# Kernel tuning notes

Hardware: AMD Instinct MI355X
Metric: run time of the kernel (lower is better)

## Reference

```python
import jax, jax.numpy as jnp
import numpy as np

TOP_K = 2


def setup_inputs() -> dict:
    key = jax.random.key(0)
    ks = jax.random.split(key, 5)
    B, S, D, F, E = 4, 2048, 1024, 2048, 8
    sd = 1.0 / np.sqrt(D)
    sf = 1.0 / np.sqrt(F)
    return {
        "hidden_states": jax.random.normal(ks[0], (B, S, D), jnp.float32),
        "router_w1": jax.random.normal(ks[1], (D, 128), jnp.float32) * sd,
        "router_w2": jax.random.normal(ks[2], (128, E), jnp.float32) * (1.0 / np.sqrt(128)),
        "W1": jax.random.normal(ks[3], (E, D, F), jnp.float32) * sd,
        "W2": jax.random.normal(ks[4], (E, F, D), jnp.float32) * sf,
    }


def reference(hidden_states, router_w1, router_w2, W1, W2):
    B, S, D = hidden_states.shape
    E = W1.shape[0]
    # --- Router: MLP -> softmax -> top-k -> renormalize ---
    router_logits = jax.nn.silu(hidden_states @ router_w1) @ router_w2  # (B,S,E)
    router_probs = jax.nn.softmax(router_logits, axis=-1)
    top_vals, top_idx = jax.lax.top_k(router_probs, TOP_K)  # (B,S,K)
    routing_weights = top_vals / jnp.sum(top_vals, axis=-1, keepdims=True)

    # --- Dispatch/combine as dense combine-weight matrix (faithful to
    # weighted scatter-add combine in _grouped_expert_forward) ---
    T = B * S
    x = hidden_states.reshape(T, D)
    idx = top_idx.reshape(T, TOP_K)
    w = routing_weights.reshape(T, TOP_K).astype(hidden_states.dtype)
    combine = jnp.zeros((T, E), hidden_states.dtype).at[
        jnp.arange(T)[:, None], idx
    ].add(w)  # (T,E)

    # --- Per-expert FFN on all tokens, then weighted combine ---
    h = jax.nn.silu(jnp.einsum("td,edf->tef", x, W1))  # (T,E,F)
    expert_out = jnp.einsum("tef,efd->ted", h, W2)      # (T,E,D)
    out = jnp.einsum("te,ted->td", combine, expert_out)
    return out.reshape(B, S, D)
```

## Files before the change

### kernel.cpp

```cpp
#include <hip/hip_runtime.h>
#include <hip/hip_bf16.h>
#include <math.h>

#define T_TOK 8192
#define E_NUM 8
#define GAP_TAU 2e-3f

typedef __attribute__((ext_vector_type(8))) short short8;
typedef __attribute__((ext_vector_type(4))) float floatx4;

__device__ __forceinline__ unsigned short f2bf(float f) {
  unsigned int u = __builtin_bit_cast(unsigned int, f);
  u += 0x7fffu + ((u >> 16) & 1u);
  return (unsigned short)(u >> 16);
}

__device__ __forceinline__ void async16(const unsigned short* g, unsigned short* l) {
  __builtin_amdgcn_global_load_lds(
      (const __attribute__((address_space(1))) void*)g,
      (__attribute__((address_space(3))) void*)l, 16, 0, 0);
}

__global__ __launch_bounds__(256) void router_fp32_kernel(
    const float* __restrict__ x, const float* __restrict__ rw1,
    const float* __restrict__ rw2,
    int* __restrict__ tok_top, float* __restrict__ tok_w,
    int* __restrict__ fix_list, int* __restrict__ fix_cnt) {
  __shared__ __align__(16) float xs[8][1024];
  __shared__ float ph[128][8];
  __shared__ float hs[8][129];
  __shared__ float ls[8][8];
  const int t = threadIdx.x;
  const int tok0 = blockIdx.x * 8;

  {
    const float4* xsrc = (const float4*)(x + (size_t)tok0 * 1024);
    float4* xd = (float4*)&xs[0][0];
#pragma unroll
    for (int i = 0; i < 8; ++i) xd[t + i * 256] = xsrc[t + i * 256];
  }
  __syncthreads();

  const int j = t & 127, h = t >> 7;
  float acc[8];
#pragma unroll
  for (int tt = 0; tt < 8; ++tt) acc[tt] = 0.f;

  const int dbeg = h * 512, dend = dbeg + 512;
#pragma unroll 2
  for (int d0 = dbeg; d0 < dend; d0 += 4) {
    float w0 = rw1[(d0 + 0) * 128 + j];
    float w1 = rw1[(d0 + 1) * 128 + j];
    float w2 = rw1[(d0 + 2) * 128 + j];
    float w3 = rw1[(d0 + 3) * 128 + j];
    float4 xv[8];
#pragma unroll
    for (int tt = 0; tt < 8; ++tt) xv[tt] = *(const float4*)&xs[tt][d0];
#pragma unroll
    for (int tt = 0; tt < 8; ++tt) {
      acc[tt] = fmaf(xv[tt].x, w0, acc[tt]);
      acc[tt] = fmaf(xv[tt].y, w1, acc[tt]);
      acc[tt] = fmaf(xv[tt].z, w2, acc[tt]);
      acc[tt] = fmaf(xv[tt].w, w3, acc[tt]);
    }
  }
  if (h == 1) {
#pragma unroll
    for (int tt = 0; tt < 8; ++tt) ph[j][tt] = acc[tt];
  }
  __syncthreads();
  if (h == 0) {
#pragma unroll
    for (int tt = 0; tt < 8; ++tt) {
      float a = acc[tt] + ph[j][tt];
      hs[tt][j] = a / (1.f + expf(-a));
    }
  }
  __syncthreads();
  if (t < 64) {
    int tt = t >> 3, e = t & 7;
    float l = 0.f;
#pragma unroll 4
    for (int jj = 0; jj < 128; ++jj) l = fmaf(hs[tt][jj], rw2[jj * 8 + e], l);
    ls[tt][e] = l;
  }
  __syncthreads();
  if (t < 8) {
    int tt = t;
    float l[8];
#pragma unroll
    for (int e = 0; e < 8; ++e) l[e] = ls[tt][e];
    int i0 = 0;
#pragma unroll
    for (int e = 1; e < 8; ++e) if (l[e] > l[i0]) i0 = e;
    int i1 = (i0 == 0) ? 1 : 0;
#pragma unroll
    for (int e = 0; e < 8; ++e) if (e != i0 && l[e] > l[i1]) i1 = e;
    float v2 = -3.4e38f;
#pragma unroll
    for (int e = 0; e < 8; ++e) if (e != i0 && e != i1 && l[e] > v2) v2 = l[e];
    float gap = l[i1] - v2;
    float p = expf(l[i1] - l[i0]);
    float w0 = 1.f / (1.f + p);
    int tok = tok0 + tt;
    tok_top[2 * tok] = i0; tok_top[2 * tok + 1] = i1;
    tok_w[2 * tok] = w0;   tok_w[2 * tok + 1] = 1.f - w0;
    if (gap < GAP_TAU) { int pos = atomicAdd(fix_cnt, 1); fix_list[pos] = tok; }
  }
}

__global__ __launch_bounds__(256) void router_fix_kernel(
    const float* __restrict__ x, const float* __restrict__ rw1,
    const float* __restrict__ rw2, const int* __restrict__ fix_list,
    const int* __restrict__ fix_cnt,
    int* __restrict__ tok_top, float* __restrict__ tok_w) {
  __shared__ __align__(16) float xs[1024];
  __shared__ double red[128];
  __shared__ double hs[128];
  __shared__ double ls[8];
  const int t = threadIdx.x;
  const int nfix = *fix_cnt;
  for (int it = blockIdx.x; it < nfix; it += gridDim.x) {
    int tok = fix_list[it];
    ((float4*)xs)[t] = ((const float4*)(x + (size_t)tok * 1024))[t];
    __syncthreads();
    const int j = t & 127, h = t >> 7;
    double a0 = 0, a1 = 0, a2 = 0, a3 = 0;
    const int dbeg = h * 512;
    for (int d0 = dbeg; d0 < dbeg + 512; d0 += 4) {
      a0 = fma((double)xs[d0 + 0], (double)rw1[(d0 + 0) * 128 + j], a0);
      a1 = fma((double)xs[d0 + 1], (double)rw1[(d0 + 1) * 128 + j], a1);
      a2 = fma((double)xs[d0 + 2], (double)rw1[(d0 + 2) * 128 + j], a2);
      a3 = fma((double)xs[d0 + 3], (double)rw1[(d0 + 3) * 128 + j], a3);
    }
    double a = (a0 + a1) + (a2 + a3);
    if (h == 1) red[j] = a;
    __syncthreads();
    if (h == 0) {
      double s = a + red[j];
      hs[j] = s / (1.0 + exp(-s));
    }
    __syncthreads();
    if (t < 8) {
      int e = t;
      double l = 0;
      for (int jj = 0; jj < 128; ++jj) l = fma(hs[jj], (double)rw2[jj * 8 + e], l);
      ls[e] = l;
    }
    __syncthreads();
    if (t == 0) {
      double l[8];
#pragma unroll
      for (int e = 0; e < 8; ++e) l[e] = ls[e];
      int i0 = 0;
#pragma unroll
      for (int e = 1; e < 8; ++e) if (l[e] > l[i0]) i0 = e;
      int i1 = (i0 == 0) ? 1 : 0;
#pragma unroll
      for (int e = 0; e < 8; ++e) if (e != i0 && l[e] > l[i1]) i1 = e;
      double p = exp(l[i1] - l[i0]);
      double w0 = 1.0 / (1.0 + p);
      tok_top[2 * tok] = i0; tok_top[2 * tok + 1] = i1;
      tok_w[2 * tok] = (float)w0; tok_w[2 * tok + 1] = (float)(1.0 - w0);
    }
    __syncthreads();
  }
}

__global__ __launch_bounds__(256) void scatter_kernel(
    const int* __restrict__ tok_top, const float* __restrict__ tok_w,
    int* __restrict__ cnt, int* __restrict__ tid_list, float* __restrict__ tw_list) {
  __shared__ int hist[8], run[8];
  const int t = threadIdx.x;
  if (t < 8) hist[t] = 0;
  __syncthreads();
  const int tok = blockIdx.x * 256 + t;
  const int e0 = tok_top[2 * tok], e1 = tok_top[2 * tok + 1];
  atomicAdd(&hist[e0], 1);
  atomicAdd(&hist[e1], 1);
  __syncthreads();
  if (t < 8) run[t] = atomicAdd(&cnt[t], hist[t]);
  __syncthreads();
  int p0 = atomicAdd(&run[e0], 1);
  tid_list[e0 * T_TOK + p0] = tok; tw_list[e0 * T_TOK + p0] = tok_w[2 * tok];
  int p1 = atomicAdd(&run[e1], 1);
  tid_list[e1 * T_TOK + p1] = tok; tw_list[e1 * T_TOK + p1] = tok_w[2 * tok + 1];
}

__global__ void prefix_kernel(const int* __restrict__ cnt, int* __restrict__ base) {
  if (threadIdx.x == 0 && blockIdx.x == 0) {
    int s = 0;
    for (int e = 0; e < E_NUM; ++e) { base[e] = s; s += cnt[e]; }
  }
}

__global__ __launch_bounds__(256) void convert_x_kernel(const float* __restrict__ in,
                                                        unsigned short* __restrict__ out) {
  size_t i = ((size_t)blockIdx.x * 256 + threadIdx.x) * 4;
  float4 v = *(const float4*)(in + i);
  ushort4 o;
  o.x = f2bf(v.x); o.y = f2bf(v.y); o.z = f2bf(v.z); o.w = f2bf(v.w);
  *(ushort4*)(out + i) = o;
}

__global__ __launch_bounds__(256) void transpose_bf16_kernel(
    const float* __restrict__ in, unsigned short* __restrict__ out, int R, int C) {
  __shared__ unsigned short tile[64][65];
  const int e = blockIdx.z;
  const int r0 = blockIdx.y * 64, c0 = blockIdx.x * 64;
  const float* src = in + (size_t)e * R * C;
  unsigned short* dst = out + (size_t)e * R * C;
  const int t = threadIdx.x;
  const int cc = (t & 15) * 4;
#pragma unroll
  for (int p = 0; p < 4; ++p) {
    int r = p * 16 + (t >> 4);
    float4 v = *(const float4*)(src + (size_t)(r0 + r) * C + c0 + cc);
    tile[cc + 0][r] = f2bf(v.x);
    tile[cc + 1][r] = f2bf(v.y);
    tile[cc + 2][r] = f2bf(v.z);
    tile[cc + 3][r] = f2bf(v.w);
  }
  __syncthreads();
#pragma unroll
  for (int p = 0; p < 4; ++p) {
    int fr = p * 16 + (t >> 4);
    ushort4 o;
    o.x = tile[fr][cc + 0]; o.y = tile[fr][cc + 1];
    o.z = tile[fr][cc + 2]; o.w = tile[fr][cc + 3];
    *(ushort4*)(dst + (size_t)(c0 + fr) * R + r0 + cc) = o;
  }
}

__global__ __launch_bounds__(256) void gemm1_kernel(
    const unsigned short* __restrict__ xb,
    const unsigned short* __restrict__ w1t,
    const int* __restrict__ cnt, const int* __restrict__ base,
    const int* __restrict__ tid_list,
    unsigned short* __restrict__ h_buf) {
  const int e = blockIdx.z;
  const int m0 = blockIdx.y * 128;
  const int n0 = blockIdx.x * 128;
  const int count = cnt[e];
  if (m0 >= count) return;
  const int bs = base[e];

  __shared__ __align__(16) unsigned short As[128 * 64];
  __shared__ __align__(16) unsigned short Bs[128 * 64];

  const int t = threadIdx.x;
  const int wv = t >> 6, lane = t & 63;
  const int quad = lane >> 4, lr = lane & 15;
  const int wm = (wv & 1) * 64, wn = (wv >> 1) * 64;
  const int lr8 = lane >> 3, lc8 = lane & 7;
  const int chunk = lc8 ^ lr8;

  const unsigned short* aptr[4];
  const unsigned short* bptr[4];
#pragma unroll
  for (int q = 0; q < 4; ++q) {
    int ar = m0 + wv * 32 + q * 8 + lr8;
    int ai = ar < count ? ar : count - 1;
    int tok = tid_list[e * T_TOK + ai];
    aptr[q] = xb + (size_t)tok * 1024 + chunk * 8;
    int br = n0 + wv * 32 + q * 8 + lr8;
    bptr[q] = w1t + ((size_t)e * 2048 + br) * 1024 + chunk * 8;
  }
  unsigned short* aldsb = &As[wv * 2048];
  unsigned short* bldsb = &Bs[wv * 2048];

  floatx4 zero = {0.f, 0.f, 0.f, 0.f};
  floatx4 acc[4][4];
#pragma unroll
  for (int i = 0; i < 4; ++i)
#pragma unroll
    for (int j = 0; j < 4; ++j) acc[i][j] = zero;

  for (int k0 = 0; k0 < 1024; k0 += 64) {
    __syncthreads();
#pragma unroll
    for (int q = 0; q < 4; ++q) {
      async16(aptr[q] + k0, aldsb + q * 512);
      async16(bptr[q] + k0, bldsb + q * 512);
    }
    __syncthreads();
#pragma unroll
    for (int ks = 0; ks < 2; ++ks) {
      short8 af[4], bfv[4];
#pragma unroll
      for (int i = 0; i < 4; ++i) {
        int r = wm + i * 16 + lr;
        int pc = (ks * 4 + quad) ^ (lr & 7);
        af[i] = *(const short8*)&As[r * 64 + pc * 8];
      }
#pragma unroll
      for (int j = 0; j < 4; ++j) {
        int r = wn + j * 16 + lr;
        int pc = (ks * 4 + quad) ^ (lr & 7);
        bfv[j] = *(const short8*)&Bs[r * 64 + pc * 8];
      }
#pragma unroll
      for (int i = 0; i < 4; ++i)
#pragma unroll
        for (int j = 0; j < 4; ++j)
          acc[i][j] = __builtin_amdgcn_mfma_f32_16x16x32_bf16(af[i], bfv[j], acc[i][j], 0, 0, 0);
    }
  }

#pragma unroll
  for (int i = 0; i < 4; ++i) {
#pragma unroll
    for (int r = 0; r < 4; ++r) {
      int grow = m0 + wm + i * 16 + quad * 4 + r;
      if (grow < count) {
        size_t rowoff = (size_t)(bs + grow) * 2048;
#pragma unroll
        for (int j = 0; j < 4; ++j) {
          float v = acc[i][j][r];
          float s = v / (1.0f + __expf(-v));
          h_buf[rowoff + n0 + wn + j * 16 + lr] = f2bf(s);
        }
      }
    }
  }
}

__global__ __launch_bounds__(256) void gemm2_kernel(
    const unsigned short* __restrict__ h_buf,
    const unsigned short* __restrict__ w2t,
    const int* __restrict__ cnt, const int* __restrict__ base,
    const int* __restrict__ tid_list, const float* __restrict__ tw_list,
    float* __restrict__ out) {
  const int e = blockIdx.z;
  const int m0 = blockIdx.y * 128;
  const int n0 = blockIdx.x * 128;
  const int count = cnt[e];
  if (m0 >= count) return;
  const int bs = base[e];

  __shared__ __align__(16) unsigned short As[128 * 64];
  __shared__ __align__(16) unsigned short Bs[128 * 64];

  const int t = threadIdx.x;
  const int wv = t >> 6, lane = t & 63;
  const int quad = lane >> 4, lr = lane & 15;
  const int wm = (wv & 1) * 64, wn = (wv >> 1) * 64;
  const int lr8 = lane >> 3, lc8 = lane & 7;
  const int chunk = lc8 ^ lr8;

  const unsigned short* aptr[4];
  const unsigned short* bptr[4];
#pragma unroll
  for (int q = 0; q < 4; ++q) {
    int ar = m0 + wv * 32 + q * 8 + lr8;
    int ai = ar < count ? ar : count - 1;
    aptr[q] = h_buf + (size_t)(bs + ai) * 2048 + chunk * 8;
    int br = n0 + wv * 32 + q * 8 + lr8;
    bptr[q] = w2t + ((size_t)e * 1024 + br) * 2048 + chunk * 8;
  }
  unsigned short* aldsb = &As[wv * 2048];
  unsigned short* bldsb = &Bs[wv * 2048];

  floatx4 zero = {0.f, 0.f, 0.f, 0.f};
  floatx4 acc[4][4];
#pragma unroll
  for (int i = 0; i < 4; ++i)
#pragma unroll
    for (int j = 0; j < 4; ++j) acc[i][j] = zero;

  for (int k0 = 0; k0 < 2048; k0 += 64) {
    __syncthreads();
#pragma unroll
    for (int q = 0; q < 4; ++q) {
      async16(aptr[q] + k0, aldsb + q * 512);
      async16(bptr[q] + k0, bldsb + q * 512);
    }
    __syncthreads();
#pragma unroll
    for (int ks = 0; ks < 2; ++ks) {
      short8 af[4], bfv[4];
#pragma unroll
      for (int i = 0; i < 4; ++i) {
        int r = wm + i * 16 + lr;
        int pc = (ks * 4 + quad) ^ (lr & 7);
        af[i] = *(const short8*)&As[r * 64 + pc * 8];
      }
#pragma unroll
      for (int j = 0; j < 4; ++j) {
        int r = wn + j * 16 + lr;
        int pc = (ks * 4 + quad) ^ (lr & 7);
        bfv[j] = *(const short8*)&Bs[r * 64 + pc * 8];
      }
#pragma unroll
      for (int i = 0; i < 4; ++i)
#pragma unroll
        for (int j = 0; j < 4; ++j)
          acc[i][j] = __builtin_amdgcn_mfma_f32_16x16x32_bf16(af[i], bfv[j], acc[i][j], 0, 0, 0);
    }
  }

#pragma unroll
  for (int i = 0; i < 4; ++i) {
#pragma unroll
    for (int r = 0; r < 4; ++r) {
      int grow = m0 + wm + i * 16 + quad * 4 + r;
      if (grow < count) {
        int tok = tid_list[e * T_TOK + grow];
        float w = tw_list[e * T_TOK + grow];
        size_t rowoff = (size_t)tok * 1024;
#pragma unroll
        for (int j = 0; j < 4; ++j) {
          unsafeAtomicAdd(&out[rowoff + n0 + wn + j * 16 + lr], acc[i][j][r] * w);
        }
      }
    }
  }
}

extern "C" void kernel_launch(void* const* d_in, const int* in_sizes, int n_in,
                              void* d_out, int out_size, void* d_ws, size_t ws_size,
                              hipStream_t stream) {
  const float* x   = (const float*)d_in[0];
  const float* rw1 = (const float*)d_in[1];
  const float* rw2 = (const float*)d_in[2];
  const float* W1  = (const float*)d_in[3];
  const float* W2  = (const float*)d_in[4];
  float* out = (float*)d_out;

  char* ws = (char*)d_ws;
  int*            cnt      = (int*)(ws + 0);
  int*            base     = (int*)(ws + 64);
  int*            fix_cnt  = (int*)(ws + 128);
  int*            tid_list = (int*)(ws + 512);
  float*          tw_list  = (float*)(ws + 262656);
  unsigned short* xb       = (unsigned short*)(ws + 524800);
  unsigned short* w1t      = (unsigned short*)(ws + 17302016);
  unsigned short* w2t      = (unsigned short*)(ws + 50856448);
  unsigned short* hbuf     = (unsigned short*)(ws + 84410880);
  int*            tok_top  = (int*)(ws + 151519744);
  float*          tok_w    = (float*)(ws + 151585280);
  int*            fix_list = (int*)(ws + 151650816);

  hipMemsetAsync(d_out, 0, (size_t)T_TOK * 1024 * 4, stream);
  hipMemsetAsync(ws, 0, 192, stream);

  hipLaunchKernelGGL(router_fp32_kernel, dim3(1024), dim3(256), 0, stream,
                     x, rw1, rw2, tok_top, tok_w, fix_list, fix_cnt);
  hipLaunchKernelGGL(router_fix_kernel, dim3(128), dim3(256), 0, stream,
                     x, rw1, rw2, fix_list, fix_cnt, tok_top, tok_w);
  hipLaunchKernelGGL(scatter_kernel, dim3(32), dim3(256), 0, stream,
                     tok_top, tok_w, cnt, tid_list, tw_list);
  hipLaunchKernelGGL(prefix_kernel, dim3(1), dim3(1), 0, stream, cnt, base);
  hipLaunchKernelGGL(convert_x_kernel, dim3(8192), dim3(256), 0, stream, x, xb);
  hipLaunchKernelGGL(transpose_bf16_kernel, dim3(32, 16, 8), dim3(256), 0, stream,
                     W1, w1t, 1024, 2048);
  hipLaunchKernelGGL(transpose_bf16_kernel, dim3(16, 32, 8), dim3(256), 0, stream,
                     W2, w2t, 2048, 1024);
  hipLaunchKernelGGL(gemm1_kernel, dim3(16, 64, 8), dim3(256), 0, stream,
                     xb, w1t, cnt, base, tid_list, hbuf);
  hipLaunchKernelGGL(gemm2_kernel, dim3(8, 64, 8), dim3(256), 0, stream,
                     hbuf, w2t, cnt, base, tid_list, tw_list, out);
}
```

Measured before the change: 565.5 us.

## Fuse bf16 conversion into router and compact GEMM grids with XCD-aware tile mapping

The fp32-to-bf16 conversion of the activations moves into the router kernel, which already loads each token row, so the separate conversion kernel and its extra read of x go away. Both grouped GEMMs switch from a 3D grid padded to the worst case per expert to a 1D grid. Each block derives its expert, M tile and N tile from a prefix sum of per-expert tile counts. The low 3 bits of the block index select an XCD band, so blocks that share tiles sit on the same XCD for L2 reuse. This removes many empty blocks that exit at once. The cost is a small per-block prefix computation, and the fixed grid sizes (2176 and 1088) must cover the total number of tiles.

```diff
diff --git a/kernel.cpp b/kernel.cpp
--- a/kernel.cpp
+++ b/kernel.cpp
@@ -21,11 +21,34 @@
       (__attribute__((address_space(3))) void*)l, 16, 0, 0);
 }
 
+__device__ __forceinline__ bool tile_map(int flat, const int* cnt, int nt_log2,
+                                         int& e, int& m0, int& n0) {
+  const int xcd = flat & 7;
+  const int idx = flat >> 3;
+  int mtp[E_NUM + 1];
+  mtp[0] = 0;
+#pragma unroll
+  for (int q = 0; q < E_NUM; ++q) mtp[q + 1] = mtp[q] + ((cnt[q] + 127) >> 7);
+  const int MT = mtp[E_NUM];
+  const int band = (MT + 7) >> 3;
+  const int i = idx >> nt_log2;
+  if (i >= band) return false;
+  const int g = xcd * band + i;
+  if (g >= MT) return false;
+  e = 0;
+#pragma unroll
+  for (int q = 0; q < E_NUM - 1; ++q) if (g >= mtp[q + 1]) e = q + 1;
+  m0 = (g - mtp[e]) << 7;
+  n0 = (idx & ((1 << nt_log2) - 1)) << 7;
+  return true;
+}
+
 __global__ __launch_bounds__(256) void router_fp32_kernel(
     const float* __restrict__ x, const float* __restrict__ rw1,
     const float* __restrict__ rw2,
     int* __restrict__ tok_top, float* __restrict__ tok_w,
-    int* __restrict__ fix_list, int* __restrict__ fix_cnt) {
+    int* __restrict__ fix_list, int* __restrict__ fix_cnt,
+    unsigned short* __restrict__ xb) {
   __shared__ __align__(16) float xs[8][1024];
   __shared__ float ph[128][8];
   __shared__ float hs[8][129];
@@ -36,8 +59,15 @@
   {
     const float4* xsrc = (const float4*)(x + (size_t)tok0 * 1024);
     float4* xd = (float4*)&xs[0][0];
-#pragma unroll
-    for (int i = 0; i < 8; ++i) xd[t + i * 256] = xsrc[t + i * 256];
+    ushort4* xbd = (ushort4*)(xb + (size_t)tok0 * 1024);
+#pragma unroll
+    for (int i = 0; i < 8; ++i) {
+      float4 v = xsrc[t + i * 256];
+      xd[t + i * 256] = v;
+      ushort4 o;
+      o.x = f2bf(v.x); o.y = f2bf(v.y); o.z = f2bf(v.z); o.w = f2bf(v.w);
+      xbd[t + i * 256] = o;
+    }
   }
   __syncthreads();
 
@@ -194,15 +224,6 @@
   }
 }
 
-__global__ __launch_bounds__(256) void convert_x_kernel(const float* __restrict__ in,
-                                                        unsigned short* __restrict__ out) {
-  size_t i = ((size_t)blockIdx.x * 256 + threadIdx.x) * 4;
-  float4 v = *(const float4*)(in + i);
-  ushort4 o;
-  o.x = f2bf(v.x); o.y = f2bf(v.y); o.z = f2bf(v.z); o.w = f2bf(v.w);
-  *(ushort4*)(out + i) = o;
-}
-
 __global__ __launch_bounds__(256) void transpose_bf16_kernel(
     const float* __restrict__ in, unsigned short* __restrict__ out, int R, int C) {
   __shared__ unsigned short tile[64][65];
@@ -238,11 +259,9 @@
     const int* __restrict__ cnt, const int* __restrict__ base,
     const int* __restrict__ tid_list,
     unsigned short* __restrict__ h_buf) {
-  const int e = blockIdx.z;
-  const int m0 = blockIdx.y * 128;
-  const int n0 = blockIdx.x * 128;
+  int e, m0, n0;
+  if (!tile_map(blockIdx.x, cnt, 4, e, m0, n0)) return;
   const int count = cnt[e];
-  if (m0 >= count) return;
   const int bs = base[e];
 
   __shared__ __align__(16) unsigned short As[128 * 64];
@@ -331,11 +350,9 @@
     const int* __restrict__ cnt, const int* __restrict__ base,
     const int* __restrict__ tid_list, const float* __restrict__ tw_list,
     float* __restrict__ out) {
-  const int e = blockIdx.z;
-  const int m0 = blockIdx.y * 128;
-  const int n0 = blockIdx.x * 128;
+  int e, m0, n0;
+  if (!tile_map(blockIdx.x, cnt, 3, e, m0, n0)) return;
   const int count = cnt[e];
-  if (m0 >= count) return;
   const int bs = base[e];
 
   __shared__ __align__(16) unsigned short As[128 * 64];
@@ -445,19 +462,18 @@
   hipMemsetAsync(ws, 0, 192, stream);
 
   hipLaunchKernelGGL(router_fp32_kernel, dim3(1024), dim3(256), 0, stream,
-                     x, rw1, rw2, tok_top, tok_w, fix_list, fix_cnt);
+                     x, rw1, rw2, tok_top, tok_w, fix_list, fix_cnt, xb);
   hipLaunchKernelGGL(router_fix_kernel, dim3(128), dim3(256), 0, stream,
                      x, rw1, rw2, fix_list, fix_cnt, tok_top, tok_w);
   hipLaunchKernelGGL(scatter_kernel, dim3(32), dim3(256), 0, stream,
                      tok_top, tok_w, cnt, tid_list, tw_list);
   hipLaunchKernelGGL(prefix_kernel, dim3(1), dim3(1), 0, stream, cnt, base);
-  hipLaunchKernelGGL(convert_x_kernel, dim3(8192), dim3(256), 0, stream, x, xb);
   hipLaunchKernelGGL(transpose_bf16_kernel, dim3(32, 16, 8), dim3(256), 0, stream,
                      W1, w1t, 1024, 2048);
   hipLaunchKernelGGL(transpose_bf16_kernel, dim3(16, 32, 8), dim3(256), 0, stream,
                      W2, w2t, 2048, 1024);
-  hipLaunchKernelGGL(gemm1_kernel, dim3(16, 64, 8), dim3(256), 0, stream,
+  hipLaunchKernelGGL(gemm1_kernel, dim3(2176), dim3(256), 0, stream,
                      xb, w1t, cnt, base, tid_list, hbuf);
-  hipLaunchKernelGGL(gemm2_kernel, dim3(8, 64, 8), dim3(256), 0, stream,
+  hipLaunchKernelGGL(gemm2_kernel, dim3(1088), dim3(256), 0, stream,
                      hbuf, w2t, cnt, base, tid_list, tw_list, out);
 }
```

Result: faster. 552.5 us (-2.3%).
